# Performance work log

Measured on AMD Instinct MI355X. Metric: run time of the kernel, lower is better.

The kernel has to match this reference:

```python
import jax, jax.numpy as jnp
import numpy as np

WIDTH = [512, 512, 512, 512]
GRID_SIZE = 5
K = 3  # spline order
GRID_RANGE = (-1.0, 1.0)
BATCH = 1024


def extend_grid(grid, k):
    # grid: (I, G+1) -> (I, G+2k+1), extend k knots on each side with uniform step h
    h = (grid[:, -1:] - grid[:, :1]) / (grid.shape[1] - 1)
    for _ in range(k):
        grid = jnp.concatenate([grid[:, :1] - h, grid, grid[:, -1:] + h], axis=1)
    return grid


def b_spline_basis(x, grid, k):
    # Cox-de Boor recursion. x: (B, I), grid: (I, G+2k+1) -> (B, I, G+k)
    xe = x[:, :, None]
    g = grid[None, :, :]
    B = ((xe >= g[:, :, :-1]) & (xe < g[:, :, 1:])).astype(x.dtype)
    for p in range(1, k + 1):
        B = ((xe - g[:, :, :-(p + 1)]) / (g[:, :, p:-1] - g[:, :, :-(p + 1)]) * B[:, :, :-1]
             + (g[:, :, p + 1:] - xe) / (g[:, :, p + 1:] - g[:, :, 1:-p]) * B[:, :, 1:])
    return B


def kan_layer(x, grid, coef, sb, sp):
    # x: (B, I); coef: (I, O, G+k); sb, sp: (I, O)
    base = jax.nn.silu(x)                              # residual b(x), (B, I)
    Bmat = b_spline_basis(x, grid, K)                  # (B, I, G+k)
    y = jnp.einsum('bik,iok->bio', Bmat, coef)         # spline curves, (B, I, O)
    post = sb[None] * base[:, :, None] + sp[None] * y  # postacts (B, I, O)
    return post.sum(axis=1)                            # (B, O)


def setup_inputs() -> dict:
    key = jax.random.key(0)
    ks = jax.random.split(key, 1 + 2 * (len(WIDTH) - 1))
    inp = {"x": jax.random.normal(ks[0], (BATCH, WIDTH[0]), dtype=jnp.float32)}
    for l, (i, o) in enumerate(zip(WIDTH[:-1], WIDTH[1:])):
        base = jnp.linspace(GRID_RANGE[0], GRID_RANGE[1], GRID_SIZE + 1, dtype=jnp.float32)
        grid = extend_grid(jnp.broadcast_to(base[None], (i, GRID_SIZE + 1)), K)
        kc, kb = ks[1 + 2 * l], ks[2 + 2 * l]
        inp[f"grid{l}"] = grid
        inp[f"coef{l}"] = jax.random.normal(kc, (i, o, GRID_SIZE + K), dtype=jnp.float32) * (0.1 / GRID_SIZE)
        inp[f"sb{l}"] = (jax.random.uniform(kb, (i, o), dtype=jnp.float32) * 2.0 - 1.0) / np.sqrt(i).astype(np.float32)
        inp[f"sp{l}"] = jnp.ones((i, o), dtype=jnp.float32) / np.sqrt(i).astype(np.float32)
    return inp


def reference(x, grid0, coef0, sb0, sp0, grid1, coef1, sb1, sp1, grid2, coef2, sb2, sp2):
    x = kan_layer(x, grid0, coef0, sb0, sp0)
    x = kan_layer(x, grid1, coef1, sb1, sp1)
    x = kan_layer(x, grid2, coef2, sb2, sp2)
    return x
```

## Files before the change

kernel.cpp:

```cpp
#include <hip/hip_runtime.h>
#include <hip/hip_bf16.h>

#define I_DIM  512
#define O_DIM  512
#define NBATCH 1024
#define NSPL   8
#define KPI    12
#define KDIM   (I_DIM * KPI)
#define NGRID  12

#define SPLITK 4
#define KSEG   (KDIM / SPLITK)
#define BK     128
#define BM     64
#define BN     64
#define NT     (KSEG / BK)

typedef __attribute__((ext_vector_type(8))) short bf16x8;
typedef __attribute__((ext_vector_type(4))) float f32x4;

__device__ __forceinline__ void gload_lds16(const __hip_bfloat16* g, __hip_bfloat16* l) {
    __builtin_amdgcn_global_load_lds(
        (const __attribute__((address_space(1))) void*)g,
        (__attribute__((address_space(3))) void*)l, 16, 0, 0);
}

__device__ __forceinline__ void features_core(float xv, const float* __restrict__ grid,
                                              __hip_bfloat16* __restrict__ dst) {
    float g[NGRID];
#pragma unroll
    for (int j = 0; j < NGRID; ++j) g[j] = grid[j];

    float h  = g[1] - g[0];
    float r1 = 1.0f / h;
    float r2 = 1.0f / (2.0f * h);
    float r3 = 1.0f / (3.0f * h);

    float B[NGRID - 1];
#pragma unroll
    for (int j = 0; j < NGRID - 1; ++j)
        B[j] = (xv >= g[j] && xv < g[j + 1]) ? 1.0f : 0.0f;

#pragma unroll
    for (int j = 0; j < NGRID - 2; ++j)
        B[j] = (xv - g[j]) * r1 * B[j] + (g[j + 2] - xv) * r1 * B[j + 1];
#pragma unroll
    for (int j = 0; j < NGRID - 3; ++j)
        B[j] = (xv - g[j]) * r2 * B[j] + (g[j + 3] - xv) * r2 * B[j + 1];
#pragma unroll
    for (int j = 0; j < NGRID - 4; ++j)
        B[j] = (xv - g[j]) * r3 * B[j] + (g[j + 4] - xv) * r3 * B[j + 1];

    float s = xv / (1.0f + __expf(-xv));
    __hip_bfloat16 shi = __float2bfloat16(s);
    __hip_bfloat16 slo = __float2bfloat16(s - __bfloat162float(shi));

    __align__(16) __hip_bfloat16 row[KPI];
#pragma unroll
    for (int k = 0; k < NSPL; ++k) row[k] = __float2bfloat16(B[k]);
    row[8]  = shi;
    row[9]  = shi;
    row[10] = slo;
    row[11] = __float2bfloat16(0.0f);

    uint2* d = (uint2*)dst;
    const uint2* srow = (const uint2*)row;
    d[0] = srow[0]; d[1] = srow[1]; d[2] = srow[2];
}

__device__ __forceinline__ void wt_row_core(const float* __restrict__ coef,
                                            const float* __restrict__ sb,
                                            const float* __restrict__ sp,
                                            int i, int o,
                                            __hip_bfloat16* __restrict__ W) {
    float sbv = sb[i * O_DIM + o];
    float spv = sp[i * O_DIM + o];
    const float* cf = coef + (size_t)(i * O_DIM + o) * NSPL;
    __align__(16) __hip_bfloat16 row[KPI];
#pragma unroll
    for (int k = 0; k < NSPL; ++k) row[k] = __float2bfloat16(spv * cf[k]);
    __hip_bfloat16 whi = __float2bfloat16(sbv);
    __hip_bfloat16 wlo = __float2bfloat16(sbv - __bfloat162float(whi));
    row[8]  = whi;
    row[9]  = wlo;
    row[10] = whi;
    row[11] = __float2bfloat16(0.0f);
    uint2* dst = (uint2*)(W + (size_t)o * KDIM + i * KPI);
    const uint2* src = (const uint2*)row;
    dst[0] = src[0]; dst[1] = src[1]; dst[2] = src[2];
}

#define WT_BLOCKS   3072
#define FEAT_BLOCKS 2048
__global__ __launch_bounds__(256)
void prep_kernel(const float* __restrict__ x0, const float* __restrict__ gr0,
                 const float* __restrict__ c0, const float* __restrict__ sb0, const float* __restrict__ sp0,
                 const float* __restrict__ c1, const float* __restrict__ sb1, const float* __restrict__ sp1,
                 const float* __restrict__ c2, const float* __restrict__ sb2, const float* __restrict__ sp2,
                 __hip_bfloat16* __restrict__ Wt,
                 __hip_bfloat16* __restrict__ F) {
    int b = blockIdx.x;
    int t = threadIdx.x;
    if (b < WT_BLOCKS) {
        int l   = b >> 10;
        int rem = b & 1023;
        int i0  = (rem & 7) * 64;
        int o0  = (rem >> 3) * 4;
        const float* coef = l == 0 ? c0  : (l == 1 ? c1  : c2);
        const float* sb   = l == 0 ? sb0 : (l == 1 ? sb1 : sb2);
        const float* sp   = l == 0 ? sp0 : (l == 1 ? sp1 : sp2);
        wt_row_core(coef, sb, sp, i0 + (t >> 2), o0 + (t & 3),
                    Wt + (size_t)l * O_DIM * KDIM);
    } else {
        int e = (b - WT_BLOCKS) * 256 + t;
        features_core(x0[e], gr0, F + (size_t)e * KPI);
    }
}

__global__ __launch_bounds__(256)
void build_features_sum(const float* __restrict__ P,
                        const float* __restrict__ grid,
                        __hip_bfloat16* __restrict__ F) {
    int e0 = (blockIdx.x * blockDim.x + threadIdx.x) * 4;
    f32x4 xv = (f32x4){0.f, 0.f, 0.f, 0.f};
#pragma unroll
    for (int s = 0; s < SPLITK; ++s) {
        f32x4 v = *(const f32x4*)&P[(size_t)s * NBATCH * I_DIM + e0];
        xv.x += v.x; xv.y += v.y; xv.z += v.z; xv.w += v.w;
    }
    features_core(xv.x, grid, F + (size_t)(e0 + 0) * KPI);
    features_core(xv.y, grid, F + (size_t)(e0 + 1) * KPI);
    features_core(xv.z, grid, F + (size_t)(e0 + 2) * KPI);
    features_core(xv.w, grid, F + (size_t)(e0 + 3) * KPI);
}

__global__ __launch_bounds__(256)
void reduce_out(const float* __restrict__ P, float* __restrict__ out) {
    int e0 = (blockIdx.x * blockDim.x + threadIdx.x) * 4;
    f32x4 v0 = (f32x4){0.f, 0.f, 0.f, 0.f};
#pragma unroll
    for (int s = 0; s < SPLITK; ++s) {
        f32x4 v = *(const f32x4*)&P[(size_t)s * NBATCH * O_DIM + e0];
        v0.x += v.x; v0.y += v.y; v0.z += v.z; v0.w += v.w;
    }
    *(f32x4*)&out[e0] = v0;
}

__global__ __launch_bounds__(256)
void gemm_kernel(const __hip_bfloat16* __restrict__ A,
                 const __hip_bfloat16* __restrict__ Wt,
                 float* __restrict__ P) {
    __shared__ __hip_bfloat16 lA[2][BM * BK];
    __shared__ __hip_bfloat16 lB[2][BN * BK];

    int bm = blockIdx.x;
    int bn = blockIdx.y;
    int ks = blockIdx.z;
    int tid = threadIdx.x;
    int lane = tid & 63;
    int wave = tid >> 6;
    int wr = (wave & 1) * 32;
    int wc = (wave >> 1) * 32;
    int q  = lane >> 4;
    int ln = lane & 15;

    f32x4 acc[2][2];
#pragma unroll
    for (int a = 0; a < 2; ++a)
#pragma unroll
        for (int b = 0; b < 2; ++b) acc[a][b] = (f32x4){0.f, 0.f, 0.f, 0.f};

    const __hip_bfloat16* Abase = A  + (size_t)(bm * BM) * KDIM + ks * KSEG;
    const __hip_bfloat16* Bbase = Wt + (size_t)(bn * BN) * KDIM + ks * KSEG;

    size_t goff[4];
    int    loff[4];
#pragma unroll
    for (int c = 0; c < 4; ++c) {
        int cc = wave * 256 + c * 64 + lane;
        int r = cc >> 4, j = (cc & 15) ^ (r & 7);
        goff[c] = (size_t)r * KDIM + j * 8;
        loff[c] = (wave * 256 + c * 64) * 8;
    }

#define STAGE(buf, kt)                                                        \
    do {                                                                      \
        _Pragma("unroll")                                                     \
        for (int c = 0; c < 4; ++c)                                           \
            gload_lds16(Abase + goff[c] + (kt), &lA[buf][loff[c]]);           \
        _Pragma("unroll")                                                     \
        for (int c = 0; c < 4; ++c)                                           \
            gload_lds16(Bbase + goff[c] + (kt), &lB[buf][loff[c]]);           \
    } while (0)

#define COMPUTE(buf)                                                          \
    do {                                                                      \
        _Pragma("unroll")                                                     \
        for (int kh = 0; kh < 4; ++kh) {                                      \
            bf16x8 af[2], bfr[2];                                             \
            _Pragma("unroll")                                                 \
            for (int rt = 0; rt < 2; ++rt) {                                  \
                int row = wr + rt * 16 + ln;                                  \
                af[rt] = *(const bf16x8*)(&lA[buf][0] + row * BK +            \
                                          (((kh * 4 + q) ^ (row & 7)) * 8));  \
            }                                                                 \
            _Pragma("unroll")                                                 \
            for (int ct = 0; ct < 2; ++ct) {                                  \
                int row = wc + ct * 16 + ln;                                  \
                bfr[ct] = *(const bf16x8*)(&lB[buf][0] + row * BK +           \
                                           (((kh * 4 + q) ^ (row & 7)) * 8)); \
            }                                                                 \
            _Pragma("unroll")                                                 \
            for (int rt = 0; rt < 2; ++rt)                                    \
                _Pragma("unroll")                                             \
                for (int ct = 0; ct < 2; ++ct)                                \
                    acc[rt][ct] = __builtin_amdgcn_mfma_f32_16x16x32_bf16(    \
                        af[rt], bfr[ct], acc[rt][ct], 0, 0, 0);               \
        }                                                                     \
    } while (0)

    STAGE(0, 0);
    STAGE(1, BK);

    for (int t = 0; t < NT; t += 2) {
        asm volatile("s_waitcnt vmcnt(8)" ::: "memory");
        __builtin_amdgcn_s_barrier();
        __builtin_amdgcn_sched_barrier(0);
        COMPUTE(0);
        __builtin_amdgcn_s_barrier();
        __builtin_amdgcn_sched_barrier(0);
        if (t + 2 < NT) STAGE(0, (t + 2) * BK);
        if (t + 3 < NT) {
            asm volatile("s_waitcnt vmcnt(8)" ::: "memory");
        } else {
            asm volatile("s_waitcnt vmcnt(0)" ::: "memory");
        }
        __builtin_amdgcn_s_barrier();
        __builtin_amdgcn_sched_barrier(0);
        COMPUTE(1);
        __builtin_amdgcn_s_barrier();
        __builtin_amdgcn_sched_barrier(0);
        if (t + 3 < NT) STAGE(1, (t + 3) * BK);
    }
#undef STAGE
#undef COMPUTE

    float* Pp = P + (size_t)ks * NBATCH * O_DIM;
    int orow = bm * BM + wr;
    int ocol = bn * BN + wc + ln;
#pragma unroll
    for (int rt = 0; rt < 2; ++rt)
#pragma unroll
        for (int ct = 0; ct < 2; ++ct)
#pragma unroll
            for (int r = 0; r < 4; ++r)
                Pp[(size_t)(orow + rt * 16 + q * 4 + r) * O_DIM + ocol + ct * 16]
                    = acc[rt][ct][r];
}

extern "C" void kernel_launch(void* const* d_in, const int* in_sizes, int n_in,
                              void* d_out, int out_size, void* d_ws, size_t ws_size,
                              hipStream_t stream) {
    const float* x0  = (const float*)d_in[0];
    const float* gr0 = (const float*)d_in[1];
    const float* c0  = (const float*)d_in[2];
    const float* sb0 = (const float*)d_in[3];
    const float* sp0 = (const float*)d_in[4];
    const float* gr1 = (const float*)d_in[5];
    const float* c1  = (const float*)d_in[6];
    const float* sb1 = (const float*)d_in[7];
    const float* sp1 = (const float*)d_in[8];
    const float* gr2 = (const float*)d_in[9];
    const float* c2  = (const float*)d_in[10];
    const float* sb2 = (const float*)d_in[11];
    const float* sp2 = (const float*)d_in[12];

    char* ws = (char*)d_ws;
    const size_t wt_bytes = (size_t)O_DIM * KDIM * sizeof(__hip_bfloat16);
    const size_t f_bytes  = (size_t)NBATCH * KDIM * sizeof(__hip_bfloat16);
    __hip_bfloat16* Wt = (__hip_bfloat16*)ws;
    __hip_bfloat16* F  = (__hip_bfloat16*)(ws + 3 * wt_bytes);
    float* P = (float*)(ws + 3 * wt_bytes + f_bytes);
    float* out = (float*)d_out;

    prep_kernel<<<WT_BLOCKS + FEAT_BLOCKS, 256, 0, stream>>>(
        x0, gr0, c0, sb0, sp0, c1, sb1, sp1, c2, sb2, sp2, Wt, F);

    gemm_kernel<<<dim3(NBATCH / BM, O_DIM / BN, SPLITK), 256, 0, stream>>>(F, Wt, P);

    build_features_sum<<<(NBATCH * I_DIM) / 1024, 256, 0, stream>>>(P, gr1, F);
    gemm_kernel<<<dim3(NBATCH / BM, O_DIM / BN, SPLITK), 256, 0, stream>>>(
        F, Wt + (size_t)O_DIM * KDIM, P);

    build_features_sum<<<(NBATCH * I_DIM) / 1024, 256, 0, stream>>>(P, gr2, F);
    gemm_kernel<<<dim3(NBATCH / BM, O_DIM / BN, SPLITK), 256, 0, stream>>>(
        F, Wt + (size_t)2 * O_DIM * KDIM, P);

    reduce_out<<<(NBATCH * O_DIM) / 1024, 256, 0, stream>>>(P, out);
}
```

Before: 169.8 us.

## Fuse split-K reduction and next-layer feature build into GEMM epilogue via counters

Each split-K GEMM block publishes its partial tile and increments a per-tile atomic counter. The last block to arrive sums the partials and either builds the next layer's bf16 spline features or writes the final output. This removes the separate reduction and feature kernels and their launches. In exchange it needs extra feature buffers and counters, and the features are computed by only a quarter of the blocks, serialised at the end of each GEMM.

```diff
diff --git a/kernel.cpp b/kernel.cpp
--- a/kernel.cpp
+++ b/kernel.cpp
@@ -23,6 +23,13 @@
     __builtin_amdgcn_global_load_lds(
         (const __attribute__((address_space(1))) void*)g,
         (__attribute__((address_space(3))) void*)l, 16, 0, 0);
+}
+
+__device__ __forceinline__ void st_dev(float* p, float v) {
+    __hip_atomic_store(p, v, __ATOMIC_RELAXED, __HIP_MEMORY_SCOPE_AGENT);
+}
+__device__ __forceinline__ float ld_dev(const float* p) {
+    return __hip_atomic_load(p, __ATOMIC_RELAXED, __HIP_MEMORY_SCOPE_AGENT);
 }
 
 __device__ __forceinline__ void features_core(float xv, const float* __restrict__ grid,
@@ -92,15 +99,19 @@
 
 #define WT_BLOCKS   3072
 #define FEAT_BLOCKS 2048
+#define NCTR        (3 * 128)
 __global__ __launch_bounds__(256)
 void prep_kernel(const float* __restrict__ x0, const float* __restrict__ gr0,
                  const float* __restrict__ c0, const float* __restrict__ sb0, const float* __restrict__ sp0,
                  const float* __restrict__ c1, const float* __restrict__ sb1, const float* __restrict__ sp1,
                  const float* __restrict__ c2, const float* __restrict__ sb2, const float* __restrict__ sp2,
                  __hip_bfloat16* __restrict__ Wt,
-                 __hip_bfloat16* __restrict__ F) {
+                 __hip_bfloat16* __restrict__ F0,
+                 int* __restrict__ ctr) {
     int b = blockIdx.x;
     int t = threadIdx.x;
+    int z = b * 256 + t;
+    if (z < NCTR) ctr[z] = 0;
     if (b < WT_BLOCKS) {
         int l   = b >> 10;
         int rem = b & 1023;
@@ -113,45 +124,22 @@
                     Wt + (size_t)l * O_DIM * KDIM);
     } else {
         int e = (b - WT_BLOCKS) * 256 + t;
-        features_core(x0[e], gr0, F + (size_t)e * KPI);
+        features_core(x0[e], gr0, F0 + (size_t)e * KPI);
     }
 }
 
 __global__ __launch_bounds__(256)
-void build_features_sum(const float* __restrict__ P,
-                        const float* __restrict__ grid,
-                        __hip_bfloat16* __restrict__ F) {
-    int e0 = (blockIdx.x * blockDim.x + threadIdx.x) * 4;
-    f32x4 xv = (f32x4){0.f, 0.f, 0.f, 0.f};
-#pragma unroll
-    for (int s = 0; s < SPLITK; ++s) {
-        f32x4 v = *(const f32x4*)&P[(size_t)s * NBATCH * I_DIM + e0];
-        xv.x += v.x; xv.y += v.y; xv.z += v.z; xv.w += v.w;
-    }
-    features_core(xv.x, grid, F + (size_t)(e0 + 0) * KPI);
-    features_core(xv.y, grid, F + (size_t)(e0 + 1) * KPI);
-    features_core(xv.z, grid, F + (size_t)(e0 + 2) * KPI);
-    features_core(xv.w, grid, F + (size_t)(e0 + 3) * KPI);
-}
-
-__global__ __launch_bounds__(256)
-void reduce_out(const float* __restrict__ P, float* __restrict__ out) {
-    int e0 = (blockIdx.x * blockDim.x + threadIdx.x) * 4;
-    f32x4 v0 = (f32x4){0.f, 0.f, 0.f, 0.f};
-#pragma unroll
-    for (int s = 0; s < SPLITK; ++s) {
-        f32x4 v = *(const f32x4*)&P[(size_t)s * NBATCH * O_DIM + e0];
-        v0.x += v.x; v0.y += v.y; v0.z += v.z; v0.w += v.w;
-    }
-    *(f32x4*)&out[e0] = v0;
-}
-
-__global__ __launch_bounds__(256)
-void gemm_kernel(const __hip_bfloat16* __restrict__ A,
-                 const __hip_bfloat16* __restrict__ Wt,
-                 float* __restrict__ P) {
+void gemm_fused(const __hip_bfloat16* __restrict__ A,
+                const __hip_bfloat16* __restrict__ Wt,
+                float* __restrict__ P,
+                const float* __restrict__ grid_next,
+                __hip_bfloat16* __restrict__ Fn,
+                float* __restrict__ out,
+                int last,
+                int* __restrict__ ctr) {
     __shared__ __hip_bfloat16 lA[2][BM * BK];
     __shared__ __hip_bfloat16 lB[2][BN * BK];
+    __shared__ int win;
 
     int bm = blockIdx.x;
     int bn = blockIdx.y;
@@ -254,8 +242,29 @@
         for (int ct = 0; ct < 2; ++ct)
 #pragma unroll
             for (int r = 0; r < 4; ++r)
-                Pp[(size_t)(orow + rt * 16 + q * 4 + r) * O_DIM + ocol + ct * 16]
-                    = acc[rt][ct][r];
+                st_dev(&Pp[(size_t)(orow + rt * 16 + q * 4 + r) * O_DIM + ocol + ct * 16],
+                       acc[rt][ct][r]);
+
+    asm volatile("s_waitcnt vmcnt(0)" ::: "memory");
+    __syncthreads();
+    if (tid == 0) win = (atomicAdd(&ctr[bm * 8 + bn], 1) == SPLITK - 1);
+    __syncthreads();
+    if (win) {
+#pragma unroll
+        for (int it = 0; it < 16; ++it) {
+            int p = it * 256 + tid;
+            int b = bm * BM + (p >> 6);
+            int o = bn * BN + (p & 63);
+            float xv = 0.f;
+#pragma unroll
+            for (int s = 0; s < SPLITK; ++s)
+                xv += ld_dev(&P[(size_t)s * NBATCH * O_DIM + (size_t)b * O_DIM + o]);
+            if (!last)
+                features_core(xv, grid_next, Fn + (size_t)b * KDIM + o * KPI);
+            else
+                out[(size_t)b * O_DIM + o] = xv;
+        }
+    }
 }
 
 extern "C" void kernel_launch(void* const* d_in, const int* in_sizes, int n_in,
@@ -279,22 +288,20 @@
     const size_t wt_bytes = (size_t)O_DIM * KDIM * sizeof(__hip_bfloat16);
     const size_t f_bytes  = (size_t)NBATCH * KDIM * sizeof(__hip_bfloat16);
     __hip_bfloat16* Wt = (__hip_bfloat16*)ws;
-    __hip_bfloat16* F  = (__hip_bfloat16*)(ws + 3 * wt_bytes);
-    float* P = (float*)(ws + 3 * wt_bytes + f_bytes);
+    __hip_bfloat16* F0 = (__hip_bfloat16*)(ws + 3 * wt_bytes);
+    __hip_bfloat16* F1 = F0 + (size_t)NBATCH * KDIM;
+    __hip_bfloat16* F2 = F1 + (size_t)NBATCH * KDIM;
+    float* P  = (float*)(ws + 3 * wt_bytes + 3 * f_bytes);
+    int* ctr  = (int*)(P + (size_t)SPLITK * NBATCH * O_DIM);
     float* out = (float*)d_out;
 
     prep_kernel<<<WT_BLOCKS + FEAT_BLOCKS, 256, 0, stream>>>(
-        x0, gr0, c0, sb0, sp0, c1, sb1, sp1, c2, sb2, sp2, Wt, F);
-
-    gemm_kernel<<<dim3(NBATCH / BM, O_DIM / BN, SPLITK), 256, 0, stream>>>(F, Wt, P);
-
-    build_features_sum<<<(NBATCH * I_DIM) / 1024, 256, 0, stream>>>(P, gr1, F);
-    gemm_kernel<<<dim3(NBATCH / BM, O_DIM / BN, SPLITK), 256, 0, stream>>>(
-        F, Wt + (size_t)O_DIM * KDIM, P);
-
-    build_features_sum<<<(NBATCH * I_DIM) / 1024, 256, 0, stream>>>(P, gr2, F);
-    gemm_kernel<<<dim3(NBATCH / BM, O_DIM / BN, SPLITK), 256, 0, stream>>>(
-        F, Wt + (size_t)2 * O_DIM * KDIM, P);
-
-    reduce_out<<<(NBATCH * O_DIM) / 1024, 256, 0, stream>>>(P, out);
-}
+        x0, gr0, c0, sb0, sp0, c1, sb1, sp1, c2, sb2, sp2, Wt, F0, ctr);
+
+    dim3 gg(NBATCH / BM, O_DIM / BN, SPLITK);
+    gemm_fused<<<gg, 256, 0, stream>>>(F0, Wt, P, gr1, F1, out, 0, ctr);
+    gemm_fused<<<gg, 256, 0, stream>>>(F1, Wt + (size_t)O_DIM * KDIM, P,
+                                       gr2, F2, out, 0, ctr + 128);
+    gemm_fused<<<gg, 256, 0, stream>>>(F2, Wt + (size_t)2 * O_DIM * KDIM, P,
+                                       nullptr, nullptr, out, 1, ctr + 256);
+}
```

After: 200.6 us. 18.1% more time.
